# Performance work log

Hardware: AMD Instinct MI355X
Metric: run time of the kernel (lower is better)

## Reference

```python
import jax, jax.numpy as jnp
import numpy as np
from jax import lax

ITER_TIME = 32
DECAY = 0.9


def setup_inputs() -> dict:
    key = jax.random.key(0)
    k1, k2, k3, k4 = jax.random.split(key, 4)
    B, D_in, N, D_out = 256, 1024, 4096, 256
    s_in = 1.0 / np.sqrt(D_in)
    s_rec = 0.5 / np.sqrt(N)  # keep recurrence stable
    s_out = 1.0 / np.sqrt(N)
    return {
        "x": jax.random.normal(k1, (B, D_in), dtype=jnp.float32),
        "W_i": jax.random.normal(k2, (D_in, N), dtype=jnp.float32) * s_in,
        "b": jnp.zeros((N,), dtype=jnp.float32),
        "W_r": jax.random.normal(k3, (N, N), dtype=jnp.float32) * s_rec,
        "W_f": jax.random.normal(k4, (N, D_out), dtype=jnp.float32) * s_out,
    }


def reference(x, W_i, b, W_r, W_f):
    # prep_input_endure: constant input drive each timestep
    i_ = x @ W_i + b  # [B, N]
    u0 = jnp.zeros_like(i_)
    r0 = jnp.zeros_like(i_)

    def step(carry, _):
        u, r = carry
        u_new = DECAY * u + i_ + r           # leaky integration of drive + recurrent feedback
        a = jax.nn.relu(u_new)               # firing rate / surrogate spike
        r_new = a @ W_r                      # recurrent N->N feedback
        f = a @ W_f                          # readout N->Y
        return (u_new, r_new), (f, u_new)

    (_, _), (fs, us) = lax.scan(step, (u0, r0), None, length=ITER_TIME)
    output = jnp.transpose(fs, (1, 0, 2))  # [B, T, output_num]
    act = jnp.transpose(us, (1, 0, 2))     # [B, T, N_num]
    return output, act
```

## Files before the change

kernel.cpp:

```cpp
#include <hip/hip_runtime.h>
#include <hip/hip_bf16.h>

#define ITER_TIME 32
#define DECAY 0.9f

typedef __attribute__((ext_vector_type(8))) short short8;
typedef __attribute__((ext_vector_type(4))) float f32x4;
typedef unsigned short ushort_t;

__global__ void conv_f32_bf16(const float* __restrict__ in,
                              __hip_bfloat16* __restrict__ out, int n) {
    int i = blockIdx.x * 256 + threadIdx.x;
    if (i < n) out[i] = __float2bfloat16(in[i]);
}

__global__ void transpose_f32_bf16(const float* __restrict__ in,
                                   __hip_bfloat16* __restrict__ out, int R,
                                   int C) {
    __shared__ float tile[32][33];
    int tx = threadIdx.x, ty = threadIdx.y;
    size_t x = blockIdx.x * 32 + tx;
    size_t y = blockIdx.y * 32 + ty;
    tile[ty][tx] = in[y * C + x];
    __syncthreads();
    size_t ox = blockIdx.y * 32 + tx;
    size_t oy = blockIdx.x * 32 + ty;
    out[oy * R + ox] = __float2bfloat16(tile[tx][ty]);
}

__global__ __launch_bounds__(256)
void gemm_splitk(const ushort_t* __restrict__ A,
                 const ushort_t* __restrict__ BT,
                 const ushort_t* __restrict__ BT2,
                 float* __restrict__ Cp,
                 float* __restrict__ C2p,
                 int K, int klen, int Nmain, int N2) {
    const int M = 256;
    __shared__ __attribute__((aligned(16))) ushort_t As[128 * 72];
    __shared__ __attribute__((aligned(16))) ushort_t Bs[128 * 72];

    int m0 = blockIdx.x * 128;
    int by = blockIdx.y;
    int ks = blockIdx.z;
    int ntile_main = Nmain >> 7;
    bool isB2 = (by >= ntile_main);
    const ushort_t* Bsrc = isB2 ? BT2 + (size_t)((by - ntile_main) * 128) * K
                                : BT + (size_t)(by * 128) * K;

    int t = threadIdx.x;
    int wave = t >> 6, lane = t & 63;
    int quad = lane >> 4, l16 = lane & 15;
    int wm = (wave >> 1) * 64, wn = (wave & 1) * 64;

    f32x4 acc[4][4];
#pragma unroll
    for (int i = 0; i < 4; i++)
#pragma unroll
        for (int j = 0; j < 4; j++) acc[i][j] = (f32x4){0.f, 0.f, 0.f, 0.f};

    int ldr = t >> 3;
    int ldc = (t & 7) * 8;

    int k0 = ks * klen;
    int iters = klen >> 6;
    for (int it = 0; it < iters; ++it) {
        int kk = k0 + it * 64;
#pragma unroll
        for (int i = 0; i < 4; ++i) {
            int r = ldr + i * 32;
            *(short8*)&As[r * 72 + ldc] =
                *(const short8*)&A[(size_t)(m0 + r) * K + kk + ldc];
            *(short8*)&Bs[r * 72 + ldc] =
                *(const short8*)&Bsrc[(size_t)r * K + kk + ldc];
        }
        __syncthreads();
#pragma unroll
        for (int kstep = 0; kstep < 2; ++kstep) {
            int ko = kstep * 32 + quad * 8;
            short8 af[4], bfr[4];
#pragma unroll
            for (int i = 0; i < 4; i++)
                af[i] = *(const short8*)&As[(wm + i * 16 + l16) * 72 + ko];
#pragma unroll
            for (int j = 0; j < 4; j++)
                bfr[j] = *(const short8*)&Bs[(wn + j * 16 + l16) * 72 + ko];
#pragma unroll
            for (int i = 0; i < 4; i++)
#pragma unroll
                for (int j = 0; j < 4; j++)
                    acc[i][j] = __builtin_amdgcn_mfma_f32_16x16x32_bf16(
                        af[i], bfr[j], acc[i][j], 0, 0, 0);
        }
        __syncthreads();
    }

#pragma unroll
    for (int i = 0; i < 4; i++) {
#pragma unroll
        for (int j = 0; j < 4; j++) {
            int gcol = by * 128 + wn + j * 16 + l16;
#pragma unroll
            for (int rr = 0; rr < 4; ++rr) {
                int grow = m0 + wm + i * 16 + quad * 4 + rr;
                float v = acc[i][j][rr];
                if (!isB2) {
                    Cp[(size_t)ks * M * Nmain + (size_t)grow * Nmain + gcol] = v;
                } else {
                    int c2 = gcol - Nmain;
                    C2p[(size_t)ks * M * N2 + (size_t)grow * N2 + c2] = v;
                }
            }
        }
    }
}

__global__ void elem_step(float* __restrict__ i_, float* __restrict__ u,
                          __hip_bfloat16* __restrict__ a,
                          const float* __restrict__ rp,
                          const float* __restrict__ fp,
                          const float* __restrict__ bias,
                          float* __restrict__ out, float* __restrict__ act,
                          int t) {
    int id = blockIdx.x * 256 + threadIdx.x;
    const int NU = 256 * 4096;
    if (id < NU) {
        if (t >= ITER_TIME) return;
        int b = id >> 12, n = id & 4095;
        float un;
        if (t == 0) {
            float iv = i_[id] + bias[n];
            i_[id] = iv;
            un = iv;
        } else {
            un = DECAY * u[id] + i_[id] + rp[id] + rp[NU + id] +
                 rp[2 * NU + id] + rp[3 * NU + id];
        }
        u[id] = un;
        float ar = un > 0.f ? un : 0.f;
        a[id] = __float2bfloat16(ar);
        act[(size_t)b * (ITER_TIME * 4096) + (size_t)t * 4096 + n] = un;
    } else {
        if (t == 0) return;
        int id2 = id - NU;
        const int NF = 256 * 256;
        int b = id2 >> 8, d = id2 & 255;
        float fv = fp[id2] + fp[NF + id2] + fp[2 * NF + id2] + fp[3 * NF + id2];
        out[(size_t)b * (ITER_TIME * 256) + (size_t)(t - 1) * 256 + d] = fv;
    }
}

extern "C" void kernel_launch(void* const* d_in, const int* in_sizes, int n_in,
                              void* d_out, int out_size, void* d_ws,
                              size_t ws_size, hipStream_t stream) {
    const float* x = (const float*)d_in[0];
    const float* Wi = (const float*)d_in[1];
    const float* bb = (const float*)d_in[2];
    const float* Wr = (const float*)d_in[3];
    const float* Wf = (const float*)d_in[4];

    float* out = (float*)d_out;
    float* act = out + (size_t)256 * ITER_TIME * 256;

    char* ws = (char*)d_ws;
    float* i_ = (float*)(ws + 0x0);
    float* u = (float*)(ws + 0x400000);
    __hip_bfloat16* a = (__hip_bfloat16*)(ws + 0x800000);
    float* rp = (float*)(ws + 0xA00000);
    float* fp = (float*)(ws + 0x1A00000);
    __hip_bfloat16* WrT = (__hip_bfloat16*)(ws + 0x1B00000);
    __hip_bfloat16* WfT = (__hip_bfloat16*)(ws + 0x3B00000);
    __hip_bfloat16* xb = (__hip_bfloat16*)(ws + 0x3D00000);
    __hip_bfloat16* WiT = (__hip_bfloat16*)(ws + 0xA00000);

    conv_f32_bf16<<<1024, 256, 0, stream>>>(x, xb, 256 * 1024);
    dim3 tb(32, 32);
    transpose_f32_bf16<<<dim3(128, 32), tb, 0, stream>>>(Wi, WiT, 1024, 4096);
    transpose_f32_bf16<<<dim3(128, 128), tb, 0, stream>>>(Wr, WrT, 4096, 4096);
    transpose_f32_bf16<<<dim3(8, 128), tb, 0, stream>>>(Wf, WfT, 4096, 256);

    gemm_splitk<<<dim3(2, 32, 1), 256, 0, stream>>>(
        (const ushort_t*)xb, (const ushort_t*)WiT, nullptr, i_, nullptr, 1024,
        1024, 4096, 256);

    for (int t = 0; t <= ITER_TIME; ++t) {
        elem_step<<<4352, 256, 0, stream>>>(i_, u, a, rp, fp, bb, out, act, t);
        if (t < ITER_TIME) {
            gemm_splitk<<<dim3(2, 34, 4), 256, 0, stream>>>(
                (const ushort_t*)a, (const ushort_t*)WrT,
                (const ushort_t*)WfT, rp, fp, 4096, 1024, 4096, 256);
        }
    }
}
```

Baseline: 1.323 ms.

## Double-buffer GEMM via direct global-to-LDS loads, raise split-K, vectorize elementwise step

The split-K GEMM now stages tiles straight into LDS with global_load_lds, using an XOR-swizzled layout and two buffers so the next K-tile loads while MFMAs run on the current one. Split-K grows from 4 to 8 when the workspace is large enough, which doubles the block count for the recurrent GEMM (68 to 136 per K-slice set) to fill more CUs. The elementwise step is vectorized to float4 and reduces a variable number of partial sums. The cost is more partial-sum traffic per timestep, and the swizzle must exactly match how the direct-to-LDS loads place data.

New measurement: 1.337 ms. No clear change (+1.0%).

```diff
diff --git a/kernel.cpp b/kernel.cpp
--- a/kernel.cpp
+++ b/kernel.cpp
@@ -6,7 +6,15 @@
 
 typedef __attribute__((ext_vector_type(8))) short short8;
 typedef __attribute__((ext_vector_type(4))) float f32x4;
+typedef __attribute__((ext_vector_type(4))) short short4v;
 typedef unsigned short ushort_t;
+typedef unsigned int u32;
+
+__device__ __forceinline__ void gload16(const ushort_t* g, ushort_t* l) {
+    __builtin_amdgcn_global_load_lds(
+        (const __attribute__((address_space(1))) u32*)g,
+        (__attribute__((address_space(3))) u32*)l, 16, 0, 0);
+}
 
 __global__ void conv_f32_bf16(const float* __restrict__ in,
                               __hip_bfloat16* __restrict__ out, int n) {
@@ -36,8 +44,8 @@
                  float* __restrict__ C2p,
                  int K, int klen, int Nmain, int N2) {
     const int M = 256;
-    __shared__ __attribute__((aligned(16))) ushort_t As[128 * 72];
-    __shared__ __attribute__((aligned(16))) ushort_t Bs[128 * 72];
+    __shared__ __attribute__((aligned(16))) ushort_t As[2][128 * 64];
+    __shared__ __attribute__((aligned(16))) ushort_t Bs[2][128 * 64];
 
     int m0 = blockIdx.x * 128;
     int by = blockIdx.y;
@@ -52,38 +60,48 @@
     int quad = lane >> 4, l16 = lane & 15;
     int wm = (wave >> 1) * 64, wn = (wave & 1) * 64;
 
+    int lr = lane >> 3;
+    int lcol = ((lane & 7) ^ lr) << 3;
+    const ushort_t* aBase = A + (size_t)(m0 + wave * 32 + lr) * K + lcol;
+    const ushort_t* bBase = Bsrc + (size_t)(wave * 32 + lr) * K + lcol;
+
     f32x4 acc[4][4];
 #pragma unroll
     for (int i = 0; i < 4; i++)
 #pragma unroll
         for (int j = 0; j < 4; j++) acc[i][j] = (f32x4){0.f, 0.f, 0.f, 0.f};
 
-    int ldr = t >> 3;
-    int ldc = (t & 7) * 8;
-
     int k0 = ks * klen;
-    int iters = klen >> 6;
-    for (int it = 0; it < iters; ++it) {
-        int kk = k0 + it * 64;
+    int nt = klen >> 6;
+
+    int swz = (l16 & 7) << 3;
+
+    auto stage = [&](int buf, int kk) {
 #pragma unroll
         for (int i = 0; i < 4; ++i) {
-            int r = ldr + i * 32;
-            *(short8*)&As[r * 72 + ldc] =
-                *(const short8*)&A[(size_t)(m0 + r) * K + kk + ldc];
-            *(short8*)&Bs[r * 72 + ldc] =
-                *(const short8*)&Bsrc[(size_t)r * K + kk + ldc];
-        }
-        __syncthreads();
+            gload16(aBase + (size_t)(i * 8) * K + kk,
+                    &As[buf][(wave * 4 + i) * 512]);
+            gload16(bBase + (size_t)(i * 8) * K + kk,
+                    &Bs[buf][(wave * 4 + i) * 512]);
+        }
+    };
+
+    stage(0, k0);
+    __syncthreads();
+    int cur = 0;
+    for (int it = 0; it < nt; ++it) {
+        if (it + 1 < nt) stage(cur ^ 1, k0 + (it + 1) * 64);
 #pragma unroll
         for (int kstep = 0; kstep < 2; ++kstep) {
             int ko = kstep * 32 + quad * 8;
+            int pc = ko ^ swz;
             short8 af[4], bfr[4];
 #pragma unroll
             for (int i = 0; i < 4; i++)
-                af[i] = *(const short8*)&As[(wm + i * 16 + l16) * 72 + ko];
+                af[i] = *(const short8*)&As[cur][(wm + i * 16 + l16) * 64 + pc];
 #pragma unroll
             for (int j = 0; j < 4; j++)
-                bfr[j] = *(const short8*)&Bs[(wn + j * 16 + l16) * 72 + ko];
+                bfr[j] = *(const short8*)&Bs[cur][(wn + j * 16 + l16) * 64 + pc];
 #pragma unroll
             for (int i = 0; i < 4; i++)
 #pragma unroll
@@ -92,6 +110,7 @@
                         af[i], bfr[j], acc[i][j], 0, 0, 0);
         }
         __syncthreads();
+        cur ^= 1;
     }
 
 #pragma unroll
@@ -120,32 +139,46 @@
                           const float* __restrict__ fp,
                           const float* __restrict__ bias,
                           float* __restrict__ out, float* __restrict__ act,
-                          int t) {
-    int id = blockIdx.x * 256 + threadIdx.x;
+                          int t, int KS) {
+    int id4 = blockIdx.x * 256 + threadIdx.x;
     const int NU = 256 * 4096;
-    if (id < NU) {
+    const int NU4 = NU / 4;
+    if (id4 < NU4) {
         if (t >= ITER_TIME) return;
+        int id = id4 * 4;
         int b = id >> 12, n = id & 4095;
-        float un;
+        f32x4 un;
         if (t == 0) {
-            float iv = i_[id] + bias[n];
-            i_[id] = iv;
+            f32x4 iv = *(f32x4*)&i_[id] + *(const f32x4*)&bias[n];
+            *(f32x4*)&i_[id] = iv;
             un = iv;
         } else {
-            un = DECAY * u[id] + i_[id] + rp[id] + rp[NU + id] +
-                 rp[2 * NU + id] + rp[3 * NU + id];
-        }
-        u[id] = un;
-        float ar = un > 0.f ? un : 0.f;
-        a[id] = __float2bfloat16(ar);
-        act[(size_t)b * (ITER_TIME * 4096) + (size_t)t * 4096 + n] = un;
+            f32x4 s = *(f32x4*)&i_[id];
+            for (int k = 0; k < KS; ++k)
+                s += *(const f32x4*)&rp[(size_t)k * NU + id];
+            un = DECAY * *(f32x4*)&u[id] + s;
+        }
+        *(f32x4*)&u[id] = un;
+        short4v av;
+#pragma unroll
+        for (int j = 0; j < 4; ++j) {
+            float ar = un[j] > 0.f ? un[j] : 0.f;
+            __hip_bfloat16 h = __float2bfloat16(ar);
+            av[j] = *(short*)&h;
+        }
+        *(short4v*)&a[id] = av;
+        *(f32x4*)&act[(size_t)b * (ITER_TIME * 4096) + (size_t)t * 4096 + n] =
+            un;
     } else {
         if (t == 0) return;
-        int id2 = id - NU;
+        int id2 = (id4 - NU4) * 4;
         const int NF = 256 * 256;
         int b = id2 >> 8, d = id2 & 255;
-        float fv = fp[id2] + fp[NF + id2] + fp[2 * NF + id2] + fp[3 * NF + id2];
-        out[(size_t)b * (ITER_TIME * 256) + (size_t)(t - 1) * 256 + d] = fv;
+        f32x4 fv = {0.f, 0.f, 0.f, 0.f};
+        for (int k = 0; k < KS; ++k)
+            fv += *(const f32x4*)&fp[(size_t)k * NF + id2];
+        *(f32x4*)&out[(size_t)b * (ITER_TIME * 256) + (size_t)(t - 1) * 256 +
+                      d] = fv;
     }
 }
 
@@ -161,15 +194,23 @@
     float* out = (float*)d_out;
     float* act = out + (size_t)256 * ITER_TIME * 256;
 
+    int KS = 8;
+    if (ws_size < (size_t)0x4E80000) KS = 4;
+
     char* ws = (char*)d_ws;
     float* i_ = (float*)(ws + 0x0);
     float* u = (float*)(ws + 0x400000);
     __hip_bfloat16* a = (__hip_bfloat16*)(ws + 0x800000);
-    float* rp = (float*)(ws + 0xA00000);
-    float* fp = (float*)(ws + 0x1A00000);
-    __hip_bfloat16* WrT = (__hip_bfloat16*)(ws + 0x1B00000);
-    __hip_bfloat16* WfT = (__hip_bfloat16*)(ws + 0x3B00000);
-    __hip_bfloat16* xb = (__hip_bfloat16*)(ws + 0x3D00000);
+    size_t off = 0xA00000;
+    float* rp = (float*)(ws + off);
+    off += (size_t)KS << 22;
+    float* fp = (float*)(ws + off);
+    off += (size_t)KS << 18;
+    __hip_bfloat16* WrT = (__hip_bfloat16*)(ws + off);
+    off += 0x2000000;
+    __hip_bfloat16* WfT = (__hip_bfloat16*)(ws + off);
+    off += 0x200000;
+    __hip_bfloat16* xb = (__hip_bfloat16*)(ws + off);
     __hip_bfloat16* WiT = (__hip_bfloat16*)(ws + 0xA00000);
 
     conv_f32_bf16<<<1024, 256, 0, stream>>>(x, xb, 256 * 1024);
@@ -182,12 +223,14 @@
         (const ushort_t*)xb, (const ushort_t*)WiT, nullptr, i_, nullptr, 1024,
         1024, 4096, 256);
 
+    int klen = 4096 / KS;
     for (int t = 0; t <= ITER_TIME; ++t) {
-        elem_step<<<4352, 256, 0, stream>>>(i_, u, a, rp, fp, bb, out, act, t);
+        elem_step<<<1088, 256, 0, stream>>>(i_, u, a, rp, fp, bb, out, act, t,
+                                            KS);
         if (t < ITER_TIME) {
-            gemm_splitk<<<dim3(2, 34, 4), 256, 0, stream>>>(
+            gemm_splitk<<<dim3(2, 34, KS), 256, 0, stream>>>(
                 (const ushort_t*)a, (const ushort_t*)WrT,
-                (const ushort_t*)WfT, rp, fp, 4096, 1024, 4096, 256);
-        }
-    }
-}
+                (const ushort_t*)WfT, rp, fp, 4096, klen, 4096, 256);
+        }
+    }
+}
```
